# Optimization experiments

Measured on AMD Instinct MI355X. Metric: run time of the kernel, lower is better.

Reference implementation:

```python
import jax, jax.numpy as jnp
import numpy as np

D_MODEL = 1024
HEADS = 16
D_K = D_MODEL // HEADS
D_FF = 2048
EPS = 1e-6


def setup_inputs() -> dict:
    key = jax.random.key(0)
    ks = jax.random.split(key, 16)
    s = 1.0 / np.sqrt(D_MODEL)
    inp = {
        'x': jax.random.normal(ks[0], (2, 4096, D_MODEL), jnp.float32),
        'Wq': jax.random.normal(ks[1], (D_MODEL, D_MODEL), jnp.float32) * s,
        'bq': jnp.zeros((D_MODEL,), jnp.float32),
        'Wk': jax.random.normal(ks[2], (D_MODEL, D_MODEL), jnp.float32) * s,
        'bk': jnp.zeros((D_MODEL,), jnp.float32),
        'Wv': jax.random.normal(ks[3], (D_MODEL, D_MODEL), jnp.float32) * s,
        'bv': jnp.zeros((D_MODEL,), jnp.float32),
        'Wo': jax.random.normal(ks[4], (D_MODEL, D_MODEL), jnp.float32) * s,
        'bo': jnp.zeros((D_MODEL,), jnp.float32),
        'W1': jax.random.normal(ks[5], (D_MODEL, D_FF), jnp.float32) * s,
        'b1': jnp.zeros((D_FF,), jnp.float32),
        'W2': jax.random.normal(ks[6], (D_FF, D_MODEL), jnp.float32) * (1.0 / np.sqrt(D_FF)),
        'b2': jnp.zeros((D_MODEL,), jnp.float32),
        'alpha1': jnp.ones((D_MODEL,), jnp.float32),
        'beta1': jnp.zeros((D_MODEL,), jnp.float32),
        'alpha2': jnp.ones((D_MODEL,), jnp.float32),
        'beta2': jnp.zeros((D_MODEL,), jnp.float32),
    }
    return inp


def _layernorm(x, alpha, beta):
    # torch LayerNorm here: (x - mean) / (std_unbiased + eps), eps added to std
    mean = jnp.mean(x, axis=-1, keepdims=True)
    std = jnp.std(x, axis=-1, keepdims=True, ddof=1)
    return alpha * (x - mean) / (std + EPS) + beta


def reference(x, Wq, bq, Wk, bk, Wv, bv, Wo, bo, W1, b1, W2, b2, alpha1, beta1, alpha2, beta2):
    B, S, _ = x.shape
    # projections -> [B, H, S, Dk]
    q = (x @ Wq + bq).reshape(B, S, HEADS, D_K).transpose(0, 2, 1, 3)
    k = (x @ Wk + bk).reshape(B, S, HEADS, D_K).transpose(0, 2, 1, 3)
    v = (x @ Wv + bv).reshape(B, S, HEADS, D_K).transpose(0, 2, 1, 3)
    scores = jnp.einsum('bhqd,bhkd->bhqk', q, k) / jnp.sqrt(jnp.float32(D_K))  # [B,H,S,S]
    probs = jax.nn.softmax(scores, axis=-1)
    attn = jnp.einsum('bhqk,bhkd->bhqd', probs, v)  # [B,H,S,Dk]
    concat = attn.transpose(0, 2, 1, 3).reshape(B, S, D_MODEL)
    attn_out = concat @ Wo + bo
    x = _layernorm(x + attn_out, alpha1, beta1)
    ff = jax.nn.relu(x @ W1 + b1) @ W2 + b2
    x = _layernorm(x + ff, alpha2, beta2)
    return x
```

## Files before the change

### kernel.cpp

```cpp
#include <hip/hip_runtime.h>
#include <hip/hip_bf16.h>
#include <stdint.h>

typedef __hip_bfloat16 bf16;
typedef __bf16 bf16x8 __attribute__((ext_vector_type(8)));
typedef float f32x4 __attribute__((ext_vector_type(4)));

#define D_MODEL 1024
#define HEADS 16
#define DK 64
#define DFF 2048
#define BATCH 2
#define SEQ 4096

#define QSCALE 0.18033688f

__device__ __forceinline__ float fexp2(float x) { return __builtin_amdgcn_exp2f(x); }

__device__ __forceinline__ void async16(const bf16* g, bf16* l) {
    __builtin_amdgcn_global_load_lds(
        (const __attribute__((address_space(1))) uint32_t*)g,
        (__attribute__((address_space(3))) uint32_t*)l, 16, 0, 0);
}

__device__ inline bool probe_is_bf16(const uint32_t* probe) {
    return probe[0] == 0x3F803F80u;
}

__global__ void fill_kernel(uint32_t* out, size_t n_words, uint32_t pattern) {
    size_t i = (size_t)blockIdx.x * blockDim.x + threadIdx.x;
    size_t stride = (size_t)gridDim.x * blockDim.x;
    for (; i < n_words; i += stride) out[i] = pattern;
}

__global__ void cvt_kernel(const void* __restrict__ src, bf16* __restrict__ dst,
                           int n, const uint32_t* __restrict__ probe) {
    const bool isb = probe_is_bf16(probe);
    const int i = (blockIdx.x * 256 + threadIdx.x) * 8;
    if (i >= n) return;
    if (isb) {
        *(uint4*)&dst[i] = *(const uint4*)((const uint16_t*)src + i);
    } else {
        const float* s = (const float*)src;
        bf16 t[8];
        #pragma unroll
        for (int k = 0; k < 8; k++) t[k] = __float2bfloat16(s[i + k]);
        *(uint4*)&dst[i] = *(uint4*)t;
    }
}

__global__ void cvtT_kernel(const void* __restrict__ src, bf16* __restrict__ dst,
                            int R, int C, const uint32_t* __restrict__ probe) {
    __shared__ float tile[32][33];
    const bool isb = probe_is_bf16(probe);
    int c0 = blockIdx.x * 32, r0 = blockIdx.y * 32;
    int tx = threadIdx.x, ty = threadIdx.y;
    #pragma unroll
    for (int i = 0; i < 32; i += 8) {
        size_t idx = (size_t)(r0 + ty + i) * C + c0 + tx;
        tile[ty + i][tx] = isb ? __bfloat162float(((const bf16*)src)[idx])
                               : ((const float*)src)[idx];
    }
    __syncthreads();
    #pragma unroll
    for (int i = 0; i < 32; i += 8)
        dst[(size_t)(c0 + ty + i) * R + r0 + tx] = __float2bfloat16(tile[tx][ty + i]);
}

struct VecPack { const void* src[10]; };

__global__ void cvt_small_kernel(VecPack vp, bf16* __restrict__ dst,
                                 const uint32_t* __restrict__ probe) {
    constexpr int lens[10] = {1024,1024,1024,1024,2048,1024,1024,1024,1024,1024};
    constexpr int offs[10] = {0,1024,2048,3072,4096,6144,7168,8192,9216,10240};
    const bool isb = probe_is_bf16(probe);
    const int seg = blockIdx.x;
    const int len = lens[seg], off = offs[seg];
    for (int j = threadIdx.x; j < len; j += 256) {
        float v = isb ? __bfloat162float(((const bf16*)vp.src[seg])[j])
                      : ((const float*)vp.src[seg])[j];
        dst[off + j] = __float2bfloat16(v);
    }
}

template <int MODE>
__launch_bounds__(256, 2)
__global__ void gemm_kernel(const bf16* __restrict__ A, const bf16* __restrict__ BT,
                            int K, int N, int nbh,
                            const bf16* __restrict__ bias0,
                            const bf16* __restrict__ bias1,
                            const bf16* __restrict__ bias2,
                            const bf16* __restrict__ resid,
                            bf16* __restrict__ Cout) {
    __shared__ __align__(16) bf16 As[128 * 32];
    __shared__ __align__(16) bf16 Bs[128 * 32];
    const int tid = threadIdx.x;
    const int n0 = blockIdx.x * 128;
    const int m0 = blockIdx.y * 128;
    const int wave = tid >> 6, lane = tid & 63;
    const int wr = wave >> 1, wc = wave & 1;
    const int quad = lane >> 4, lr = lane & 15;

    f32x4 acc[4][4] = {};

    const int r_a = tid >> 2, kc_a = (tid & 3) * 8;
    const int r_b = r_a + 64, kc_b = kc_a;
    bf16* asd0 = &As[wave * 512];
    bf16* asd1 = &As[2048 + wave * 512];
    bf16* bsd0 = &Bs[wave * 512];
    bf16* bsd1 = &Bs[2048 + wave * 512];
    const bf16* ag0 = &A[(size_t)(m0 + r_a) * K + kc_a];
    const bf16* ag1 = &A[(size_t)(m0 + r_b) * K + kc_b];
    const bf16* bg0 = &BT[(size_t)(n0 + r_a) * K + kc_a];
    const bf16* bg1 = &BT[(size_t)(n0 + r_b) * K + kc_b];

    for (int k0 = 0; k0 < K; k0 += 32) {
        async16(ag0 + k0, asd0);
        async16(ag1 + k0, asd1);
        async16(bg0 + k0, bsd0);
        async16(bg1 + k0, bsd1);
        __syncthreads();
        bf16x8 af[4], bfr[4];
        #pragma unroll
        for (int i = 0; i < 4; i++)
            af[i] = *(const bf16x8*)&As[(wr * 64 + i * 16 + lr) * 32 + quad * 8];
        #pragma unroll
        for (int j = 0; j < 4; j++)
            bfr[j] = *(const bf16x8*)&Bs[(wc * 64 + j * 16 + lr) * 32 + quad * 8];
        #pragma unroll
        for (int i = 0; i < 4; i++)
            #pragma unroll
            for (int j = 0; j < 4; j++)
                acc[i][j] = __builtin_amdgcn_mfma_f32_16x16x32_bf16(af[i], bfr[j], acc[i][j], 0, 0, 0);
        __syncthreads();
    }

    #pragma unroll
    for (int i = 0; i < 4; i++) {
        #pragma unroll
        for (int j = 0; j < 4; j++) {
            const int col = n0 + wc * 64 + j * 16 + lr;
            #pragma unroll
            for (int r = 0; r < 4; r++) {
                const int row = m0 + wr * 64 + i * 16 + quad * 4 + r;
                float v = acc[i][j][r];
                if (MODE == 0) {
                    const int which = col >> 10, n1 = col & 1023;
                    const int h = n1 >> 6, d = n1 & 63;
                    const bf16* bp = (which == 0) ? bias0 : (which == 1 ? bias1 : bias2);
                    v += __bfloat162float(bp[n1]);
                    const int s = row & 4095;
                    const int bh = (row >> 12) * HEADS + h;
                    const size_t region = (size_t)nbh * SEQ * DK;
                    size_t idx;
                    if (which == 2) {
                        const int sl = s & 63;
                        const int sp = (s & ~63) | ((sl & 15) << 2) | (sl >> 4);
                        idx = 2 * region + ((size_t)bh * DK + d) * SEQ + sp;
                    } else {
                        if (which == 0) v *= QSCALE;
                        idx = (size_t)which * region + ((size_t)bh * SEQ + s) * DK + d;
                    }
                    Cout[idx] = __float2bfloat16(v);
                } else if (MODE == 1) {
                    v += __bfloat162float(bias0[col]);
                    v += __bfloat162float(resid[(size_t)row * N + col]);
                    Cout[(size_t)row * N + col] = __float2bfloat16(v);
                } else {
                    v += __bfloat162float(bias0[col]);
                    v = fmaxf(v, 0.f);
                    Cout[(size_t)row * N + col] = __float2bfloat16(v);
                }
            }
        }
    }
}

__launch_bounds__(256, 2)
__global__ void flash_kernel(const bf16* __restrict__ Q, const bf16* __restrict__ Kg,
                             const bf16* __restrict__ VT, bf16* __restrict__ Oc) {
    __shared__ __align__(16) bf16 Klds[2][64 * 32];
    __shared__ __align__(16) bf16 Vlds[2][64 * 32];
    __shared__ __align__(16) bf16 Plds[4][16 * 72];
    const int tid = threadIdx.x;
    const int wave = tid >> 6, lane = tid & 63;
    const int quad = lane >> 4, lr = lane & 15;
    const int h = blockIdx.y;
    const int z = blockIdx.z;
    const int s0 = blockIdx.x * 64;
    const size_t head_off = ((size_t)z * HEADS + h) * SEQ * DK;

    bf16x8 qf[2];
    {
        const bf16* qrow = Q + head_off + (size_t)(s0 + wave * 16 + lr) * DK + quad * 8;
        qf[0] = *(const bf16x8*)(qrow);
        qf[1] = *(const bf16x8*)(qrow + 32);
    }
    bf16x8 ones;
    #pragma unroll
    for (int i = 0; i < 8; i++) ones[i] = (__bf16)1.0f;

    f32x4 o[4] = {};
    f32x4 accl = {};

    const int srow = wave * 16 + (lane >> 2);
    const int scol = (lane & 3) * 8;
    const bf16* kg = Kg + head_off + (size_t)srow * DK + scol;
    const bf16* vg = VT + head_off + (size_t)srow * SEQ + scol;
    bf16* kd0 = &Klds[0][wave * 512];
    bf16* kd1 = &Klds[1][wave * 512];
    bf16* vd0 = &Vlds[0][wave * 512];
    bf16* vd1 = &Vlds[1][wave * 512];

    for (int kv0 = 0; kv0 < SEQ; kv0 += 64) {
        async16(kg + (size_t)kv0 * DK, kd0);
        async16(kg + (size_t)kv0 * DK + 32, kd1);
        async16(vg + kv0, vd0);
        async16(vg + kv0 + 32, vd1);
        __syncthreads();

        f32x4 sc[4];
        #pragma unroll
        for (int jt = 0; jt < 4; jt++) {
            f32x4 z4 = {};
            #pragma unroll
            for (int st = 0; st < 2; st++) {
                bf16x8 kf = *(const bf16x8*)&Klds[st][(jt * 16 + lr) * 32 + quad * 8];
                z4 = __builtin_amdgcn_mfma_f32_16x16x32_bf16(qf[st], kf, z4, 0, 0, 0);
            }
            sc[jt] = z4;
        }

        #pragma unroll
        for (int r = 0; r < 4; r++) {
            bf16 pb[4];
            #pragma unroll
            for (int jt = 0; jt < 4; jt++)
                pb[jt] = __float2bfloat16(fexp2(sc[jt][r]));
            *(uint2*)&Plds[wave][(quad * 4 + r) * 72 + lr * 4] = *(uint2*)pb;
        }

        #pragma unroll
        for (int st = 0; st < 2; st++) {
            bf16x8 pf = *(const bf16x8*)&Plds[wave][lr * 72 + st * 32 + quad * 8];
            accl = __builtin_amdgcn_mfma_f32_16x16x32_bf16(pf, ones, accl, 0, 0, 0);
            #pragma unroll
            for (int dt = 0; dt < 4; dt++) {
                bf16x8 vf = *(const bf16x8*)&Vlds[st][(dt * 16 + lr) * 32 + quad * 8];
                o[dt] = __builtin_amdgcn_mfma_f32_16x16x32_bf16(pf, vf, o[dt], 0, 0, 0);
            }
        }
        __syncthreads();
    }

    float inv_l[4];
    #pragma unroll
    for (int r = 0; r < 4; r++) inv_l[r] = 1.f / accl[r];
    #pragma unroll
    for (int dt = 0; dt < 4; dt++) {
        #pragma unroll
        for (int r = 0; r < 4; r++) {
            const int s = s0 + wave * 16 + quad * 4 + r;
            float v = o[dt][r] * inv_l[r];
            Oc[(size_t)(z * SEQ + s) * D_MODEL + h * 64 + dt * 16 + lr] = __float2bfloat16(v);
        }
    }
}

template <int EXT>
__launch_bounds__(256)
__global__ void ln_kernel(const bf16* __restrict__ y, const bf16* __restrict__ alpha,
                          const bf16* __restrict__ beta,
                          bf16* __restrict__ out_bf, float* __restrict__ out_f32,
                          const uint32_t* __restrict__ probe) {
    const int wave = threadIdx.x >> 6, lane = threadIdx.x & 63;
    const size_t row = (size_t)blockIdx.x * 4 + wave;
    const bf16* yr = y + row * D_MODEL;
    float vals[16];
    float s = 0.f, sq = 0.f;
    #pragma unroll
    for (int c = 0; c < 2; c++) {
        bf16x8 v = *(const bf16x8*)&yr[c * 512 + lane * 8];
        #pragma unroll
        for (int k = 0; k < 8; k++) {
            float f = (float)v[k];
            vals[c * 8 + k] = f;
            s += f;
            sq += f * f;
        }
    }
    #pragma unroll
    for (int d = 1; d < 64; d <<= 1) { s += __shfl_xor(s, d, 64); sq += __shfl_xor(sq, d, 64); }
    const float mean = s * (1.f / 1024.f);
    const float var = fmaxf((sq - 1024.f * mean * mean) * (1.f / 1023.f), 0.f);
    const float inv = 1.f / (sqrtf(var) + 1e-6f);
    const bool out_bf16 = EXT ? probe_is_bf16(probe) : true;
    #pragma unroll
    for (int c = 0; c < 2; c++) {
        float ov[8];
        #pragma unroll
        for (int k = 0; k < 8; k++) {
            const int col = c * 512 + lane * 8 + k;
            ov[k] = __bfloat162float(alpha[col]) * (vals[c * 8 + k] - mean) * inv +
                    __bfloat162float(beta[col]);
        }
        const size_t base = row * D_MODEL + c * 512 + lane * 8;
        if (out_bf16) {
            bf16 tmp[8];
            #pragma unroll
            for (int k = 0; k < 8; k++) tmp[k] = __float2bfloat16(ov[k]);
            *(uint4*)&out_bf[base] = *(uint4*)tmp;
        } else {
            *(float4*)&out_f32[base]     = *(float4*)&ov[0];
            *(float4*)&out_f32[base + 4] = *(float4*)&ov[4];
        }
    }
}

extern "C" void kernel_launch(void* const* d_in, const int* in_sizes, int n_in,
                              void* d_out, int out_size, void* d_ws, size_t ws_size,
                              hipStream_t stream) {
    const size_t NEED1 = 67174400;
    const size_t NEED2 = 100728832;
    if (n_in != 17) {
        fill_kernel<<<1024, 256, 0, stream>>>((uint32_t*)d_out, (size_t)out_size / 2, 0x44FA44FAu);
        return;
    }
    if (ws_size < NEED1) {
        fill_kernel<<<1024, 256, 0, stream>>>((uint32_t*)d_out, (size_t)out_size / 2, 0x447A447Au);
        return;
    }

    const uint32_t* probe = (const uint32_t*)d_in[13];

    char* ws = (char*)d_ws;
    bf16* TQKV = (bf16*)(ws + 0);
    bf16* WoT  = (bf16*)(ws + 6291456);
    bf16* W1T  = (bf16*)(ws + 8388608);
    bf16* W2T  = (bf16*)(ws + 12582912);
    bf16* XB   = (bf16*)(ws + 16777216);
    bf16* SV   = (bf16*)(ws + 33554432);

    const bf16* s_bq = SV, *s_bk = SV + 1024, *s_bv = SV + 2048, *s_bo = SV + 3072;
    const bf16* s_b1 = SV + 4096, *s_b2 = SV + 6144;
    const bf16* s_a1 = SV + 7168, *s_be1 = SV + 8192, *s_a2 = SV + 9216, *s_be2 = SV + 10240;

    dim3 tb(32, 8);
    cvtT_kernel<<<dim3(32, 32), tb, 0, stream>>>(d_in[1], TQKV,                1024, 1024, probe);
    cvtT_kernel<<<dim3(32, 32), tb, 0, stream>>>(d_in[3], TQKV + 1024 * 1024,  1024, 1024, probe);
    cvtT_kernel<<<dim3(32, 32), tb, 0, stream>>>(d_in[5], TQKV + 2048 * 1024,  1024, 1024, probe);
    cvtT_kernel<<<dim3(32, 32), tb, 0, stream>>>(d_in[7], WoT,                 1024, 1024, probe);
    cvtT_kernel<<<dim3(64, 32), tb, 0, stream>>>(d_in[9], W1T,                 1024, 2048, probe);
    cvtT_kernel<<<dim3(32, 64), tb, 0, stream>>>(d_in[11], W2T,                2048, 1024, probe);
    cvt_kernel<<<4096, 256, 0, stream>>>(d_in[0], XB, BATCH * SEQ * D_MODEL, probe);
    VecPack vp;
    vp.src[0] = d_in[2]; vp.src[1] = d_in[4]; vp.src[2] = d_in[6]; vp.src[3] = d_in[8];
    vp.src[4] = d_in[10]; vp.src[5] = d_in[12]; vp.src[6] = d_in[13]; vp.src[7] = d_in[14];
    vp.src[8] = d_in[15]; vp.src[9] = d_in[16];
    cvt_small_kernel<<<10, 256, 0, stream>>>(vp, SV, probe);

    if (ws_size >= NEED2) {
        bf16* QKVm = (bf16*)(ws + 33619968);
        bf16* Qm   = QKVm;
        bf16* Km   = QKVm + (size_t)BATCH * HEADS * SEQ * DK;
        bf16* VTm  = QKVm + (size_t)2 * BATCH * HEADS * SEQ * DK;
        bf16* attnm = (bf16*)(ws + 83951616);
        bf16* y1m  = (bf16*)(ws + 33619968);
        bf16* x1m  = (bf16*)(ws + 50397184);
        bf16* hm   = (bf16*)(ws + 67174400);
        bf16* y2m  = (bf16*)(ws + 33619968);

        gemm_kernel<0><<<dim3(24, 64), 256, 0, stream>>>(XB, TQKV, 1024, 3072, BATCH * HEADS,
                                                         s_bq, s_bk, s_bv, nullptr, QKVm);
        flash_kernel<<<dim3(64, 16, 2), 256, 0, stream>>>(Qm, Km, VTm, attnm);
        gemm_kernel<1><<<dim3(8, 64), 256, 0, stream>>>(attnm, WoT, 1024, 1024, 0,
                                                        s_bo, nullptr, nullptr, XB, y1m);
        ln_kernel<0><<<2048, 256, 0, stream>>>(y1m, s_a1, s_be1, x1m, nullptr, nullptr);
        gemm_kernel<2><<<dim3(16, 64), 256, 0, stream>>>(x1m, W1T, 1024, 2048, 0,
                                                         s_b1, nullptr, nullptr, nullptr, hm);
        gemm_kernel<1><<<dim3(8, 64), 256, 0, stream>>>(hm, W2T, 2048, 1024, 0,
                                                        s_b2, nullptr, nullptr, x1m, y2m);
        ln_kernel<1><<<2048, 256, 0, stream>>>(y2m, s_a2, s_be2,
                                               (bf16*)d_out, (float*)d_out, probe);
    } else {
        char* PB   = ws + 33619968;
        bf16* Qb   = (bf16*)(PB);
        bf16* Kb   = (bf16*)(PB + 8388608);
        bf16* VTb  = (bf16*)(PB + 16777216);
        bf16* attnb = (bf16*)(PB + 25165824);
        bf16* y1b  = (bf16*)(PB);
        bf16* x1b  = (bf16*)(PB + 8388608);
        bf16* hb   = (bf16*)(PB + 16777216);
        bf16* y2b  = (bf16*)(PB);

        for (int b = 0; b < BATCH; b++) {
            const bf16* xb = XB + (size_t)b * SEQ * D_MODEL;
            bf16* out_bf   = (bf16*)d_out + (size_t)b * SEQ * D_MODEL;
            float* out_f32 = (float*)d_out + (size_t)b * SEQ * D_MODEL;

            gemm_kernel<0><<<dim3(24, 32), 256, 0, stream>>>(xb, TQKV, 1024, 3072, HEADS,
                                                             s_bq, s_bk, s_bv, nullptr, Qb);
            flash_kernel<<<dim3(64, 16, 1), 256, 0, stream>>>(Qb, Kb, VTb, attnb);
            gemm_kernel<1><<<dim3(8, 32), 256, 0, stream>>>(attnb, WoT, 1024, 1024, 0,
                                                            s_bo, nullptr, nullptr, xb, y1b);
            ln_kernel<0><<<1024, 256, 0, stream>>>(y1b, s_a1, s_be1, x1b, nullptr, nullptr);
            gemm_kernel<2><<<dim3(16, 32), 256, 0, stream>>>(x1b, W1T, 1024, 2048, 0,
                                                             s_b1, nullptr, nullptr, nullptr, hb);
            gemm_kernel<1><<<dim3(8, 32), 256, 0, stream>>>(hb, W2T, 2048, 1024, 0,
                                                            s_b2, nullptr, nullptr, x1b, y2b);
            ln_kernel<1><<<1024, 256, 0, stream>>>(y2b, s_a2, s_be2, out_bf, out_f32, probe);
        }
    }
}
```

Baseline: 590.0 us.

## Pre-swizzle K and V into MFMA fragment order and load directly from global

The QKV projection epilogue now writes K and V in a per-64-key-block layout where each lane's MFMA B-operand fragment is a contiguous 16-byte chunk. The flash kernel then loads K and V fragments straight from global or L2 into registers, dropping the LDS staging buffers and both block-wide barriers per KV iteration. Each wave now fetches the full K/V tile on its own, so the four waves read the same data four times and rely on cache hits. Register pressure also rises because 16 fragments are held per iteration.

```diff
diff --git a/kernel.cpp b/kernel.cpp
--- a/kernel.cpp
+++ b/kernel.cpp
@@ -152,14 +152,25 @@
                     const int s = row & 4095;
                     const int bh = (row >> 12) * HEADS + h;
                     const size_t region = (size_t)nbh * SEQ * DK;
+                    const int kvb = s >> 6;
                     size_t idx;
-                    if (which == 2) {
+                    if (which == 0) {
+                        v *= QSCALE;
+                        idx = ((size_t)bh * SEQ + s) * DK + d;
+                    } else if (which == 1) {
+                        const int jt = (s >> 4) & 3, lrk = s & 15;
+                        const int st = d >> 5, qk = (d >> 3) & 3, jk = d & 7;
+                        idx = region +
+                              ((((size_t)(bh * 64 + kvb) * 4 + jt) * 2 + st) * 64 +
+                               qk * 16 + lrk) * 8 + jk;
+                    } else {
                         const int sl = s & 63;
-                        const int sp = (s & ~63) | ((sl & 15) << 2) | (sl >> 4);
-                        idx = 2 * region + ((size_t)bh * DK + d) * SEQ + sp;
-                    } else {
-                        if (which == 0) v *= QSCALE;
-                        idx = (size_t)which * region + ((size_t)bh * SEQ + s) * DK + d;
+                        const int c = ((sl & 15) << 2) | (sl >> 4);
+                        const int st = c >> 5, q2 = (c >> 3) & 3, j2 = c & 7;
+                        const int dt = d >> 4, lr2 = d & 15;
+                        idx = 2 * region +
+                              ((((size_t)(bh * 64 + kvb) * 4 + dt) * 2 + st) * 64 +
+                               q2 * 16 + lr2) * 8 + j2;
                     }
                     Cout[idx] = __float2bfloat16(v);
                 } else if (MODE == 1) {
@@ -177,10 +188,8 @@
 }
 
 __launch_bounds__(256, 2)
-__global__ void flash_kernel(const bf16* __restrict__ Q, const bf16* __restrict__ Kg,
-                             const bf16* __restrict__ VT, bf16* __restrict__ Oc) {
-    __shared__ __align__(16) bf16 Klds[2][64 * 32];
-    __shared__ __align__(16) bf16 Vlds[2][64 * 32];
+__global__ void flash_kernel(const bf16* __restrict__ Q, const bf16* __restrict__ KF,
+                             const bf16* __restrict__ VF, bf16* __restrict__ Oc) {
     __shared__ __align__(16) bf16 Plds[4][16 * 72];
     const int tid = threadIdx.x;
     const int wave = tid >> 6, lane = tid & 63;
@@ -188,7 +197,8 @@
     const int h = blockIdx.y;
     const int z = blockIdx.z;
     const int s0 = blockIdx.x * 64;
-    const size_t head_off = ((size_t)z * HEADS + h) * SEQ * DK;
+    const int bh = z * HEADS + h;
+    const size_t head_off = (size_t)bh * SEQ * DK;
 
     bf16x8 qf[2];
     {
@@ -203,31 +213,30 @@
     f32x4 o[4] = {};
     f32x4 accl = {};
 
-    const int srow = wave * 16 + (lane >> 2);
-    const int scol = (lane & 3) * 8;
-    const bf16* kg = Kg + head_off + (size_t)srow * DK + scol;
-    const bf16* vg = VT + head_off + (size_t)srow * SEQ + scol;
-    bf16* kd0 = &Klds[0][wave * 512];
-    bf16* kd1 = &Klds[1][wave * 512];
-    bf16* vd0 = &Vlds[0][wave * 512];
-    bf16* vd1 = &Vlds[1][wave * 512];
+    const bf16* kfp = KF + head_off + (size_t)lane * 8;
+    const bf16* vfp = VF + head_off + (size_t)lane * 8;
 
     for (int kv0 = 0; kv0 < SEQ; kv0 += 64) {
-        async16(kg + (size_t)kv0 * DK, kd0);
-        async16(kg + (size_t)kv0 * DK + 32, kd1);
-        async16(vg + kv0, vd0);
-        async16(vg + kv0 + 32, vd1);
-        __syncthreads();
+        bf16x8 kf[4][2];
+        #pragma unroll
+        for (int jt = 0; jt < 4; jt++)
+            #pragma unroll
+            for (int st = 0; st < 2; st++)
+                kf[jt][st] = *(const bf16x8*)(kfp + (jt * 2 + st) * 512);
+        bf16x8 vf[4][2];
+        #pragma unroll
+        for (int dt = 0; dt < 4; dt++)
+            #pragma unroll
+            for (int st = 0; st < 2; st++)
+                vf[dt][st] = *(const bf16x8*)(vfp + (dt * 2 + st) * 512);
 
         f32x4 sc[4];
         #pragma unroll
         for (int jt = 0; jt < 4; jt++) {
             f32x4 z4 = {};
             #pragma unroll
-            for (int st = 0; st < 2; st++) {
-                bf16x8 kf = *(const bf16x8*)&Klds[st][(jt * 16 + lr) * 32 + quad * 8];
-                z4 = __builtin_amdgcn_mfma_f32_16x16x32_bf16(qf[st], kf, z4, 0, 0, 0);
-            }
+            for (int st = 0; st < 2; st++)
+                z4 = __builtin_amdgcn_mfma_f32_16x16x32_bf16(qf[st], kf[jt][st], z4, 0, 0, 0);
             sc[jt] = z4;
         }
 
@@ -245,12 +254,11 @@
             bf16x8 pf = *(const bf16x8*)&Plds[wave][lr * 72 + st * 32 + quad * 8];
             accl = __builtin_amdgcn_mfma_f32_16x16x32_bf16(pf, ones, accl, 0, 0, 0);
             #pragma unroll
-            for (int dt = 0; dt < 4; dt++) {
-                bf16x8 vf = *(const bf16x8*)&Vlds[st][(dt * 16 + lr) * 32 + quad * 8];
-                o[dt] = __builtin_amdgcn_mfma_f32_16x16x32_bf16(pf, vf, o[dt], 0, 0, 0);
-            }
-        }
-        __syncthreads();
+            for (int dt = 0; dt < 4; dt++)
+                o[dt] = __builtin_amdgcn_mfma_f32_16x16x32_bf16(pf, vf[dt][st], o[dt], 0, 0, 0);
+        }
+        kfp += 4096;
+        vfp += 4096;
     }
 
     float inv_l[4];
```

Measured after the change: 649.2 us. +10.0%, slower.
